# Kernel optimization log

Measured on AMD Instinct MI355X. Metric: run time of the kernel, lower is better.

Reference implementation:

```python
import jax, jax.numpy as jnp
import numpy as np

B, S, D, H = 2, 2048, 1024, 16
HD = D // H  # head_dim = 64


def setup_inputs() -> dict:
    key = jax.random.key(0)
    ks = jax.random.split(key, 12)
    scale = 1.0 / np.sqrt(D)
    inp = {
        "query": jax.random.normal(ks[0], (B, S, D), jnp.float32),
        "key": jax.random.normal(ks[1], (B, S, D), jnp.float32),
        "value": jax.random.normal(ks[2], (B, S, D), jnp.float32),
        # causal mask, True = masked out; shape [B, q_len, k_len]
        "mask": jnp.broadcast_to(
            jnp.triu(jnp.ones((S, S), jnp.bool_), k=1), (B, S, S)
        ),
        "Wq": jax.random.normal(ks[3], (D, D), jnp.float32) * scale,
        "bq": jnp.zeros((D,), jnp.float32),
        "Wk": jax.random.normal(ks[4], (D, D), jnp.float32) * scale,
        "bk": jnp.zeros((D,), jnp.float32),
        "Wv": jax.random.normal(ks[5], (D, D), jnp.float32) * scale,
        "bv": jnp.zeros((D,), jnp.float32),
        "Wo": jax.random.normal(ks[6], (D, D), jnp.float32) * scale,
        "bo": jnp.zeros((D,), jnp.float32),
    }
    return inp


def _split_heads(x):
    b, s, _ = x.shape
    return x.reshape(b, s, H, HD).transpose(0, 2, 1, 3)  # [B,H,S,HD]


def reference(query, key, value, mask, Wq, bq, Wk, bk, Wv, bv, Wo, bo):
    # Linear layers use torch convention: y = x @ W.T + b, W is [out, in]
    q = _split_heads(query @ Wq.T + bq)
    k = _split_heads(key @ Wk.T + bk)
    v = _split_heads(value @ Wv.T + bv)
    scores = jnp.einsum("bhqd,bhkd->bhqk", q, k) / jnp.sqrt(jnp.float32(HD))
    # normalized mask [B,1,q,k]; True means masked
    scores = jnp.where(mask[:, None, :, :], jnp.finfo(scores.dtype).min, scores)
    attn = jax.nn.softmax(scores, axis=-1)  # dropout is identity in eval
    ctx = jnp.einsum("bhqk,bhkd->bhqd", attn, v)
    merged = ctx.transpose(0, 2, 1, 3).reshape(query.shape[0], -1, D)
    out = merged @ Wo.T + bo
    return out
```

## Files before the change

kernel.cpp:

```cpp
#include <hip/hip_runtime.h>

#define B_ 2
#define S_ 2048
#define D_ 1024
#define H_ 16
#define HD_ 64
#define M_ (B_ * S_)

typedef __bf16 bf16x8 __attribute__((ext_vector_type(8)));
typedef float f32x4 __attribute__((ext_vector_type(4)));

__device__ inline unsigned short f2bf(float f) {
    unsigned int u = __builtin_bit_cast(unsigned int, f);
    u += 0x7fffu + ((u >> 16) & 1u);
    return (unsigned short)(u >> 16);
}

__device__ inline void async_ld16(const unsigned short* g, unsigned short* l) {
    __builtin_amdgcn_global_load_lds(
        (const __attribute__((address_space(1))) unsigned int*)g,
        (__attribute__((address_space(3))) unsigned int*)l, 16, 0, 0);
}

template <int CTRL>
__device__ inline float dpp_mov(float v) {
    return __builtin_bit_cast(float,
        __builtin_amdgcn_update_dpp(0, __builtin_bit_cast(int, v), CTRL, 0xF, 0xF, true));
}
__device__ inline float row_max16(float v) {
    v = fmaxf(v, dpp_mov<0xB1>(v));
    v = fmaxf(v, dpp_mov<0x4E>(v));
    v = fmaxf(v, dpp_mov<0x141>(v));
    v = fmaxf(v, dpp_mov<0x140>(v));
    return v;
}
__device__ inline float row_sum16(float v) {
    v += dpp_mov<0xB1>(v);
    v += dpp_mov<0x4E>(v);
    v += dpp_mov<0x141>(v);
    v += dpp_mov<0x140>(v);
    return v;
}

__global__ __launch_bounds__(256) void cvt3(const float* __restrict__ a, const float* __restrict__ b,
                                            const float* __restrict__ c,
                                            unsigned short* __restrict__ oa, unsigned short* __restrict__ ob,
                                            unsigned short* __restrict__ oc) {
    const float* in = (blockIdx.y == 0) ? a : (blockIdx.y == 1) ? b : c;
    unsigned short* out = (blockIdx.y == 0) ? oa : (blockIdx.y == 1) ? ob : oc;
    int i = (blockIdx.x * 256 + threadIdx.x) * 4;
    float4 v = *(const float4*)(in + i);
    ushort4 o;
    o.x = f2bf(v.x); o.y = f2bf(v.y); o.z = f2bf(v.z); o.w = f2bf(v.w);
    *(ushort4*)(out + i) = o;
}

__global__ __launch_bounds__(256) void cvt4(const float* __restrict__ a, const float* __restrict__ b,
                                            const float* __restrict__ c, const float* __restrict__ d,
                                            unsigned short* __restrict__ oa, unsigned short* __restrict__ ob,
                                            unsigned short* __restrict__ oc, unsigned short* __restrict__ od) {
    int z = blockIdx.y;
    const float* in = (z == 0) ? a : (z == 1) ? b : (z == 2) ? c : d;
    unsigned short* out = (z == 0) ? oa : (z == 1) ? ob : (z == 2) ? oc : od;
    int i = (blockIdx.x * 256 + threadIdx.x) * 4;
    float4 v = *(const float4*)(in + i);
    ushort4 o;
    o.x = f2bf(v.x); o.y = f2bf(v.y); o.z = f2bf(v.z); o.w = f2bf(v.w);
    *(ushort4*)(out + i) = o;
}

__device__ inline void gemm_compute(const unsigned short* __restrict__ A,
                                    const unsigned short* __restrict__ W,
                                    int K, int m0, int n0,
                                    unsigned short* As, unsigned short* Bs,
                                    f32x4 acc[4][4]) {
    const int t = threadIdx.x;
    const int lane = t & 63, wave = t >> 6;
    const int ml = lane & 15, quad = lane >> 4;
    const int wr = (wave >> 1) * 64, wc = (wave & 1) * 64;
    const int lrow = lane >> 3;
    const int gchunk = (lane & 7) ^ lrow;

    const f32x4 zero = {0.f, 0.f, 0.f, 0.f};
    for (int i = 0; i < 4; i++)
        for (int j = 0; j < 4; j++) acc[i][j] = zero;

    for (int kt = 0; kt < K; kt += 64) {
        for (int i = 0; i < 4; i++) {
            int r = wave * 32 + i * 8;
            async_ld16(A + (size_t)(m0 + r + lrow) * K + kt + gchunk * 8, As + r * 64);
            async_ld16(W + (size_t)(n0 + r + lrow) * K + kt + gchunk * 8, Bs + r * 64);
        }
        __syncthreads();
        for (int kk = 0; kk < 2; ++kk) {
            bf16x8 af[4], bfr[4];
            for (int i = 0; i < 4; i++)
                af[i] = *(const bf16x8*)(As + (wr + i * 16 + ml) * 64 + (((kk * 4 + quad) ^ (ml & 7)) << 3));
            for (int j = 0; j < 4; j++)
                bfr[j] = *(const bf16x8*)(Bs + (wc + j * 16 + ml) * 64 + (((kk * 4 + quad) ^ (ml & 7)) << 3));
            for (int i = 0; i < 4; i++)
                for (int j = 0; j < 4; j++)
                    acc[i][j] = __builtin_amdgcn_mfma_f32_16x16x32_bf16(af[i], bfr[j], acc[i][j], 0, 0, 0);
        }
        __syncthreads();
    }
}

__global__ __launch_bounds__(256) void gemm_qkv(
    const unsigned short* __restrict__ xq, const unsigned short* __restrict__ xk,
    const unsigned short* __restrict__ xv,
    const unsigned short* __restrict__ wq, const unsigned short* __restrict__ wk,
    const unsigned short* __restrict__ wv,
    const float* __restrict__ bq, const float* __restrict__ bk, const float* __restrict__ bv,
    unsigned short* __restrict__ oq, unsigned short* __restrict__ ok,
    unsigned short* __restrict__ ov) {
    __shared__ unsigned short As[128 * 64], Bs[128 * 64];
    const unsigned short *A, *W;
    const float* bias;
    unsigned short* out;
    int z = blockIdx.z;
    if (z == 0) { A = xq; W = wq; bias = bq; out = oq; }
    else if (z == 1) { A = xk; W = wk; bias = bk; out = ok; }
    else { A = xv; W = wv; bias = bv; out = ov; }

    int m0 = blockIdx.y * 128, n0 = blockIdx.x * 128;
    f32x4 acc[4][4];
    gemm_compute(A, W, D_, m0, n0, As, Bs, acc);

    const int t = threadIdx.x, lane = t & 63, wave = t >> 6;
    const int ml = lane & 15, quad = lane >> 4;
    const int wr = (wave >> 1) * 64, wc = (wave & 1) * 64;
    if (z < 2) {
        for (int i = 0; i < 4; i++)
            for (int j = 0; j < 4; j++) {
                int n = n0 + wc + j * 16 + ml;
                float bb = bias[n];
                int h = n >> 6, d = n & 63;
                for (int rg = 0; rg < 4; rg++) {
                    int m = m0 + wr + i * 16 + quad * 4 + rg;
                    int b = m >> 11, s = m & 2047;
                    out[(((size_t)(b * H_ + h)) * S_ + s) * 64 + d] = f2bf(acc[i][j][rg] + bb);
                }
            }
    } else {
        for (int i = 0; i < 4; i++)
            for (int j = 0; j < 4; j++) {
                int n = n0 + wc + j * 16 + ml;
                float bb = bias[n];
                int h = n >> 6, d = n & 63;
                int m = m0 + wr + i * 16 + quad * 4;
                int b = m >> 11, s = m & 2047;
                ushort4 pk;
                pk.x = f2bf(acc[i][j][0] + bb);
                pk.y = f2bf(acc[i][j][1] + bb);
                pk.z = f2bf(acc[i][j][2] + bb);
                pk.w = f2bf(acc[i][j][3] + bb);
                *(ushort4*)(out + ((size_t)(b * H_ + h) * 64 + d) * S_ + s) = pk;
            }
    }
}

__global__ __launch_bounds__(256) void gemm_out(const unsigned short* __restrict__ A,
                                                const unsigned short* __restrict__ W,
                                                const float* __restrict__ bias,
                                                float* __restrict__ out) {
    __shared__ unsigned short As[128 * 64], Bs[128 * 64];
    int m0 = blockIdx.y * 128, n0 = blockIdx.x * 128;
    f32x4 acc[4][4];
    gemm_compute(A, W, D_, m0, n0, As, Bs, acc);

    const int t = threadIdx.x, lane = t & 63, wave = t >> 6;
    const int ml = lane & 15, quad = lane >> 4;
    const int wr = (wave >> 1) * 64, wc = (wave & 1) * 64;
    for (int i = 0; i < 4; i++)
        for (int j = 0; j < 4; j++) {
            int n = n0 + wc + j * 16 + ml;
            float bb = bias[n];
            for (int rg = 0; rg < 4; rg++) {
                int m = m0 + wr + i * 16 + quad * 4 + rg;
                out[(size_t)m * D_ + n] = acc[i][j][rg] + bb;
            }
        }
}

__global__ __launch_bounds__(256, 2) void attn_kernel(const unsigned short* __restrict__ qh,
                                                      const unsigned short* __restrict__ kh,
                                                      const unsigned short* __restrict__ vt,
                                                      unsigned short* __restrict__ ctx) {
    __shared__ unsigned short Ks[2][128 * 64];
    __shared__ unsigned short Vs[2][64 * 128];
    __shared__ unsigned short Ps[64 * 128];

    const int qb = 31 - (blockIdx.x >> 5);
    const int bh = blockIdx.x & 31;
    const size_t base = (size_t)bh * S_ * 64;
    const int t = threadIdx.x, lane = t & 63, wave = t >> 6;
    const int ml = lane & 15, quad = lane >> 4;
    const int lrow = lane >> 3;
    const int gchunk = (lane & 7) ^ lrow;
    const int vrow = lane >> 4;
    const int q0 = qb * 64;

    bf16x8 qf[2];
    {
        int qrow = q0 + wave * 16 + ml;
        qf[0] = *(const bf16x8*)(qh + base + (size_t)qrow * 64 + quad * 8);
        qf[1] = *(const bf16x8*)(qh + base + (size_t)qrow * 64 + 32 + quad * 8);
    }

    const f32x4 zero = {0.f, 0.f, 0.f, 0.f};
    f32x4 acc[4];
    for (int j = 0; j < 4; j++) acc[j] = zero;
    float m_i[4], l_i[4];
    for (int rg = 0; rg < 4; rg++) { m_i[rg] = -INFINITY; l_i[rg] = 0.f; }

    const int ntiles = (qb + 2) >> 1;

    auto issue_tile = [&](int kt, int bb) {
        for (int i = 0; i < 4; i++) {
            int r = wave * 32 + i * 8;
            async_ld16(kh + base + (size_t)(kt * 128 + r + lrow) * 64 + gchunk * 8,
                       Ks[bb] + r * 64);
            int dd = wave * 16 + i * 4;
            int d = dd + vrow;
            async_ld16(vt + base + (size_t)d * S_ + kt * 128 + (((lane & 15) ^ (d & 15)) << 3),
                       Vs[bb] + dd * 128);
        }
    };

    issue_tile(0, 0);
    __syncthreads();

    for (int kt = 0; kt < ntiles; kt++) {
        const int buf = kt & 1;
        if (kt + 1 < ntiles) issue_tile(kt + 1, buf ^ 1);

        f32x4 sacc[8];
        for (int n = 0; n < 8; n++) sacc[n] = zero;
        for (int n = 0; n < 8; n++)
            for (int kk = 0; kk < 2; kk++) {
                bf16x8 kf = *(const bf16x8*)(Ks[buf] + (n * 16 + ml) * 64 +
                                             (((kk * 4 + quad) ^ (ml & 7)) << 3));
                sacc[n] = __builtin_amdgcn_mfma_f32_16x16x32_bf16(qf[kk], kf, sacc[n], 0, 0, 0);
            }

        const float scl = 0.125f;
        const bool last = (kt == ntiles - 1);
        for (int n = 0; n < 8; n++)
            for (int rg = 0; rg < 4; rg++) {
                float sv = sacc[n][rg] * scl;
                if (last) {
                    int kidx = kt * 128 + n * 16 + ml;
                    int qidx = q0 + wave * 16 + quad * 4 + rg;
                    if (kidx > qidx) sv = -3.0e38f;
                }
                sacc[n][rg] = sv;
            }

        float alpha[4];
        for (int rg = 0; rg < 4; rg++) {
            float v = sacc[0][rg];
            for (int n = 1; n < 8; n++) v = fmaxf(v, sacc[n][rg]);
            v = row_max16(v);
            float mo = m_i[rg];
            float mc = fmaxf(mo, v);
            alpha[rg] = __expf(mo - mc);
            m_i[rg] = mc;
        }
        float rsum[4] = {0.f, 0.f, 0.f, 0.f};
        for (int n = 0; n < 8; n++)
            for (int rg = 0; rg < 4; rg++) {
                float p = __expf(sacc[n][rg] - m_i[rg]);
                sacc[n][rg] = p;
                rsum[rg] += p;
            }
        for (int rg = 0; rg < 4; rg++) {
            float v = row_sum16(rsum[rg]);
            l_i[rg] = l_i[rg] * alpha[rg] + v;
            for (int j = 0; j < 4; j++) acc[j][rg] *= alpha[rg];
        }

        const int prow0 = wave * 16;
        for (int n = 0; n < 8; n++)
            for (int rg = 0; rg < 4; rg++) {
                int row = prow0 + quad * 4 + rg;
                int col = n * 16 + ml;
                int c = col >> 3;
                Ps[row * 128 + (((c ^ (row & 7)) & 15) << 3) + (col & 7)] = f2bf(sacc[n][rg]);
            }

        for (int kk = 0; kk < 4; kk++) {
            bf16x8 pf = *(const bf16x8*)(Ps + (prow0 + ml) * 128 +
                                         (((kk * 4 + quad) ^ (ml & 7)) << 3));
            for (int j = 0; j < 4; j++) {
                bf16x8 vf = *(const bf16x8*)(Vs[buf] + (j * 16 + ml) * 128 +
                                             (((kk * 4 + quad) ^ ml) << 3));
                acc[j] = __builtin_amdgcn_mfma_f32_16x16x32_bf16(pf, vf, acc[j], 0, 0, 0);
            }
        }

        __syncthreads();
    }

    int b = bh >> 4, h = bh & 15;
    for (int j = 0; j < 4; j++) {
        int d = j * 16 + ml;
        for (int rg = 0; rg < 4; rg++) {
            int srow = q0 + wave * 16 + quad * 4 + rg;
            float val = acc[j][rg] / l_i[rg];
            ctx[((size_t)(b * S_ + srow)) * D_ + h * 64 + d] = f2bf(val);
        }
    }
}

extern "C" void kernel_launch(void* const* d_in, const int* in_sizes, int n_in,
                              void* d_out, int out_size, void* d_ws, size_t ws_size,
                              hipStream_t stream) {
    const float* query = (const float*)d_in[0];
    const float* key_ = (const float*)d_in[1];
    const float* value = (const float*)d_in[2];
    const float* Wq = (const float*)d_in[4];
    const float* bq = (const float*)d_in[5];
    const float* Wk = (const float*)d_in[6];
    const float* bk = (const float*)d_in[7];
    const float* Wv = (const float*)d_in[8];
    const float* bv = (const float*)d_in[9];
    const float* Wo = (const float*)d_in[10];
    const float* bo = (const float*)d_in[11];
    float* out = (float*)d_out;

    const size_t XE = (size_t)M_ * D_;
    const size_t WE = (size_t)D_ * D_;
    char* ws = (char*)d_ws;
    unsigned short* xq = (unsigned short*)ws; ws += XE * 2;
    unsigned short* xk = (unsigned short*)ws; ws += XE * 2;
    unsigned short* xv = (unsigned short*)ws; ws += XE * 2;
    unsigned short* wqb = (unsigned short*)ws; ws += WE * 2;
    unsigned short* wkb = (unsigned short*)ws; ws += WE * 2;
    unsigned short* wvb = (unsigned short*)ws; ws += WE * 2;
    unsigned short* wob = (unsigned short*)ws; ws += WE * 2;
    unsigned short* qh = (unsigned short*)ws; ws += XE * 2;
    unsigned short* kh = (unsigned short*)ws; ws += XE * 2;
    unsigned short* vt = (unsigned short*)ws; ws += XE * 2;
    unsigned short* ctx = (unsigned short*)ws; ws += XE * 2;

    cvt3<<<dim3(XE / 1024, 3), 256, 0, stream>>>(query, key_, value, xq, xk, xv);
    cvt4<<<dim3(WE / 1024, 4), 256, 0, stream>>>(Wq, Wk, Wv, Wo, wqb, wkb, wvb, wob);

    gemm_qkv<<<dim3(D_ / 128, M_ / 128, 3), 256, 0, stream>>>(
        xq, xk, xv, wqb, wkb, wvb, bq, bk, bv, qh, kh, vt);

    attn_kernel<<<dim3(1024), 256, 0, stream>>>(qh, kh, vt, ctx);

    gemm_out<<<dim3(D_ / 128, M_ / 128), 256, 0, stream>>>(ctx, wob, bo, out);
}
```

Measured before the change: 261.5 us.

## Double-buffer GEMM LDS tiles and merge conversion kernels into one launch

The shared GEMM loop now keeps two LDS buffers for each of A and W. It issues the async global-to-LDS loads for the next K tile before computing on the current one, so load latency can overlap the MFMA work instead of stalling at a barrier every iteration. The two fp32-to-bf16 conversion kernels become a single launch with a bounds check per tensor, removing one kernel launch. The cost is twice the LDS per GEMM block (64 KB), which may lower GEMM occupancy. Correctness depends on the end-of-iteration barrier also waiting for the in-flight async loads.

Measured after the change: 256.7 us. No clear change (-1.9%).

```diff
diff --git a/kernel.cpp b/kernel.cpp
--- a/kernel.cpp
+++ b/kernel.cpp
@@ -42,37 +42,32 @@
     return v;
 }
 
-__global__ __launch_bounds__(256) void cvt3(const float* __restrict__ a, const float* __restrict__ b,
-                                            const float* __restrict__ c,
-                                            unsigned short* __restrict__ oa, unsigned short* __restrict__ ob,
-                                            unsigned short* __restrict__ oc) {
-    const float* in = (blockIdx.y == 0) ? a : (blockIdx.y == 1) ? b : c;
-    unsigned short* out = (blockIdx.y == 0) ? oa : (blockIdx.y == 1) ? ob : oc;
+__global__ __launch_bounds__(256) void cvt_all(
+    const float* __restrict__ i0, const float* __restrict__ i1, const float* __restrict__ i2,
+    const float* __restrict__ i3, const float* __restrict__ i4, const float* __restrict__ i5,
+    const float* __restrict__ i6,
+    unsigned short* __restrict__ o0, unsigned short* __restrict__ o1, unsigned short* __restrict__ o2,
+    unsigned short* __restrict__ o3, unsigned short* __restrict__ o4, unsigned short* __restrict__ o5,
+    unsigned short* __restrict__ o6, int nbig, int nsmall) {
+    int z = blockIdx.y;
+    const float* in = (z == 0) ? i0 : (z == 1) ? i1 : (z == 2) ? i2 : (z == 3) ? i3
+                     : (z == 4) ? i4 : (z == 5) ? i5 : i6;
+    unsigned short* out = (z == 0) ? o0 : (z == 1) ? o1 : (z == 2) ? o2 : (z == 3) ? o3
+                         : (z == 4) ? o4 : (z == 5) ? o5 : o6;
+    int n = (z < 3) ? nbig : nsmall;
     int i = (blockIdx.x * 256 + threadIdx.x) * 4;
+    if (i >= n) return;
     float4 v = *(const float4*)(in + i);
     ushort4 o;
     o.x = f2bf(v.x); o.y = f2bf(v.y); o.z = f2bf(v.z); o.w = f2bf(v.w);
     *(ushort4*)(out + i) = o;
 }
 
-__global__ __launch_bounds__(256) void cvt4(const float* __restrict__ a, const float* __restrict__ b,
-                                            const float* __restrict__ c, const float* __restrict__ d,
-                                            unsigned short* __restrict__ oa, unsigned short* __restrict__ ob,
-                                            unsigned short* __restrict__ oc, unsigned short* __restrict__ od) {
-    int z = blockIdx.y;
-    const float* in = (z == 0) ? a : (z == 1) ? b : (z == 2) ? c : d;
-    unsigned short* out = (z == 0) ? oa : (z == 1) ? ob : (z == 2) ? oc : od;
-    int i = (blockIdx.x * 256 + threadIdx.x) * 4;
-    float4 v = *(const float4*)(in + i);
-    ushort4 o;
-    o.x = f2bf(v.x); o.y = f2bf(v.y); o.z = f2bf(v.z); o.w = f2bf(v.w);
-    *(ushort4*)(out + i) = o;
-}
-
 __device__ inline void gemm_compute(const unsigned short* __restrict__ A,
                                     const unsigned short* __restrict__ W,
                                     int K, int m0, int n0,
-                                    unsigned short* As, unsigned short* Bs,
+                                    unsigned short* As0, unsigned short* As1,
+                                    unsigned short* Bs0, unsigned short* Bs1,
                                     f32x4 acc[4][4]) {
     const int t = threadIdx.x;
     const int lane = t & 63, wave = t >> 6;
@@ -85,13 +80,25 @@
     for (int i = 0; i < 4; i++)
         for (int j = 0; j < 4; j++) acc[i][j] = zero;
 
-    for (int kt = 0; kt < K; kt += 64) {
+    const int niter = K >> 6;
+
+    auto issue = [&](int kt, unsigned short* As, unsigned short* Bs) {
+        int k0 = kt << 6;
         for (int i = 0; i < 4; i++) {
             int r = wave * 32 + i * 8;
-            async_ld16(A + (size_t)(m0 + r + lrow) * K + kt + gchunk * 8, As + r * 64);
-            async_ld16(W + (size_t)(n0 + r + lrow) * K + kt + gchunk * 8, Bs + r * 64);
-        }
-        __syncthreads();
+            async_ld16(A + (size_t)(m0 + r + lrow) * K + k0 + gchunk * 8, As + r * 64);
+            async_ld16(W + (size_t)(n0 + r + lrow) * K + k0 + gchunk * 8, Bs + r * 64);
+        }
+    };
+
+    issue(0, As0, Bs0);
+    __syncthreads();
+
+    for (int kt = 0; kt < niter; kt++) {
+        unsigned short* As = (kt & 1) ? As1 : As0;
+        unsigned short* Bs = (kt & 1) ? Bs1 : Bs0;
+        if (kt + 1 < niter) issue(kt + 1, (kt & 1) ? As0 : As1, (kt & 1) ? Bs0 : Bs1);
+
         for (int kk = 0; kk < 2; ++kk) {
             bf16x8 af[4], bfr[4];
             for (int i = 0; i < 4; i++)
@@ -114,7 +121,7 @@
     const float* __restrict__ bq, const float* __restrict__ bk, const float* __restrict__ bv,
     unsigned short* __restrict__ oq, unsigned short* __restrict__ ok,
     unsigned short* __restrict__ ov) {
-    __shared__ unsigned short As[128 * 64], Bs[128 * 64];
+    __shared__ unsigned short As0[128 * 64], As1[128 * 64], Bs0[128 * 64], Bs1[128 * 64];
     const unsigned short *A, *W;
     const float* bias;
     unsigned short* out;
@@ -125,7 +132,7 @@
 
     int m0 = blockIdx.y * 128, n0 = blockIdx.x * 128;
     f32x4 acc[4][4];
-    gemm_compute(A, W, D_, m0, n0, As, Bs, acc);
+    gemm_compute(A, W, D_, m0, n0, As0, As1, Bs0, Bs1, acc);
 
     const int t = threadIdx.x, lane = t & 63, wave = t >> 6;
     const int ml = lane & 15, quad = lane >> 4;
@@ -164,10 +171,10 @@
                                                 const unsigned short* __restrict__ W,
                                                 const float* __restrict__ bias,
                                                 float* __restrict__ out) {
-    __shared__ unsigned short As[128 * 64], Bs[128 * 64];
+    __shared__ unsigned short As0[128 * 64], As1[128 * 64], Bs0[128 * 64], Bs1[128 * 64];
     int m0 = blockIdx.y * 128, n0 = blockIdx.x * 128;
     f32x4 acc[4][4];
-    gemm_compute(A, W, D_, m0, n0, As, Bs, acc);
+    gemm_compute(A, W, D_, m0, n0, As0, As1, Bs0, Bs1, acc);
 
     const int t = threadIdx.x, lane = t & 63, wave = t >> 6;
     const int ml = lane & 15, quad = lane >> 4;
@@ -344,8 +351,9 @@
     unsigned short* vt = (unsigned short*)ws; ws += XE * 2;
     unsigned short* ctx = (unsigned short*)ws; ws += XE * 2;
 
-    cvt3<<<dim3(XE / 1024, 3), 256, 0, stream>>>(query, key_, value, xq, xk, xv);
-    cvt4<<<dim3(WE / 1024, 4), 256, 0, stream>>>(Wq, Wk, Wv, Wo, wqb, wkb, wvb, wob);
+    cvt_all<<<dim3(XE / 1024, 7), 256, 0, stream>>>(
+        query, key_, value, Wq, Wk, Wv, Wo,
+        xq, xk, xv, wqb, wkb, wvb, wob, (int)XE, (int)WE);
 
     gemm_qkv<<<dim3(D_ / 128, M_ / 128, 3), 256, 0, stream>>>(
         xq, xk, xv, wqb, wkb, wvb, bq, bk, bv, qh, kh, vt);
```
